# Performance work log

Measured on AMD Instinct MI355X. Metric: run time of the kernel, lower is better.

## Reference

```python
import jax, jax.numpy as jnp
import numpy as np

TEMP = 0.1
EPS = 1e-12  # F.normalize eps


def setup_inputs() -> dict:
    key = jax.random.key(0)
    k1, k2 = jax.random.split(key)
    B, C, N = 8, 128, 4096
    features = jax.random.normal(k1, (B, C, N), dtype=jnp.float32)
    labels_all = jax.random.randint(k2, (B, N), 0, 16, dtype=jnp.int32)
    return {"features": features, "labels_all": labels_all}


def _per_cloud_loss(features_map, labels):
    # features_map: [C, N], labels: [N]
    v = features_map.T  # [N, C]
    v = v / jnp.maximum(jnp.linalg.norm(v, axis=1, keepdims=True), EPS)
    dp = jnp.exp(jnp.matmul(v, v.T) / TEMP)  # [N, N]
    n = dp.shape[0]
    # remove diagonal (dot_products - diag(diagonal))
    dp = dp * (1.0 - jnp.eye(n, dtype=dp.dtype))
    mask = labels[:, None] == labels[None, :]  # [N, N]
    positives = jnp.sum(jnp.where(mask, dp, 0.0), axis=1)
    negatives = jnp.sum(jnp.where(mask, 0.0, dp), axis=1)
    deviation = -jnp.log(positives / (positives + negatives))
    return jnp.mean(deviation)


def reference(features, labels_all):
    # features: [B, C, N], labels_all: [B, N]
    losses = jax.vmap(_per_cloud_loss)(features, labels_all)  # [B]
    return jnp.mean(losses)
```

## Files before the change

### kernel.cpp

```cpp
#include <hip/hip_runtime.h>
#include <hip/hip_bf16.h>
#include <math.h>

#define BATCH 8
#define NPTS 4096
#define CH 128
#define CTG 4
#define ROWS 128
#define CHUNK 32
#define NCHUNK (NPTS / (CTG * CHUNK))
#define NBUF 3

#define SQRT_TEMP_LOG2E 3.79828256f

typedef __attribute__((ext_vector_type(4))) float    f32x4;
typedef __attribute__((ext_vector_type(4))) int      i32x4;
typedef __attribute__((ext_vector_type(8))) short    bf16x8;
typedef __attribute__((ext_vector_type(4))) _Float16 f16x4;

typedef __attribute__((address_space(3))) unsigned int lds_uint;
typedef __attribute__((address_space(1))) const unsigned int gbl_uint;

__device__ __forceinline__ void load_lds16(const void* g, const void* l) {
    __builtin_amdgcn_global_load_lds((gbl_uint*)g, (lds_uint*)l, 16, 0, 0);
}

__device__ __forceinline__ float fast_exp2(float x) {
    return __builtin_amdgcn_exp2f(x);
}

__device__ __forceinline__ f32x4 mfma16(f16x4 a, f16x4 b, f32x4 c) {
#if __has_builtin(__builtin_amdgcn_mfma_f32_16x16x16f16)
    return __builtin_amdgcn_mfma_f32_16x16x16f16(a, b, c, 0, 0, 0);
#else
    f32x4 d = c;
    asm volatile("v_mfma_f32_16x16x16_f16 %0, %1, %2, %0"
                 : "+v"(d) : "v"(a), "v"(b));
    return d;
#endif
}

__global__ __launch_bounds__(256) void normalize_kernel(
    const float* __restrict__ f, __hip_bfloat16* __restrict__ vn,
    float* __restrict__ pos, float* __restrict__ neg, float* __restrict__ out)
{
    const int blk = blockIdx.x;
    const int b = blk >> 6;
    const int n0 = (blk & 63) * 64;
    const int nl = threadIdx.x & 63;
    const int cg = threadIdx.x >> 6;
    const float* base = f + (size_t)b * CH * NPTS + (size_t)(cg * 32) * NPTS
                          + n0 + nl;

    __shared__ float red[4][64];
    __shared__ float scl[64];
    __shared__ short ostage[64 * CH];

    float ss = 0.0f;
    #pragma unroll
    for (int c = 0; c < 32; c++) {
        float v = base[(size_t)c * NPTS];
        ss += v * v;
    }
    red[cg][nl] = ss;
    __syncthreads();
    if (cg == 0) {
        float s = red[0][nl] + red[1][nl] + red[2][nl] + red[3][nl];
        scl[nl] = SQRT_TEMP_LOG2E / fmaxf(sqrtf(s), 1e-12f);
    }
    __syncthreads();
    const float scale = scl[nl];

    #pragma unroll
    for (int k = 0; k < 4; k++) {
        union { __hip_bfloat16 h[8]; uint4 u; } pk;
        #pragma unroll
        for (int j = 0; j < 8; j++) {
            float v = base[(size_t)(k * 8 + j) * NPTS] * scale;
            pk.h[j] = __float2bfloat16(v);
        }
        const int ch8 = cg * 4 + k;
        const int phys = (nl << 4) | (ch8 ^ (nl & 15));
        *(uint4*)&ostage[phys * 8] = pk.u;
    }
    __syncthreads();

    __hip_bfloat16* ob = vn + ((size_t)b * NPTS + n0) * CH;
    const int t = threadIdx.x;
    #pragma unroll
    for (int it = 0; it < 4; it++) {
        const int L = it * 256 + t;
        const int pt = L >> 4, c8 = L & 15;
        const int phys = (pt << 4) | (c8 ^ (pt & 15));
        *(uint4*)(ob + (size_t)L * 8) = *(const uint4*)&ostage[phys * 8];
    }

    if (cg == 0) pos[b * NPTS + n0 + nl] = 0.0f;
    else if (cg == 1) neg[b * NPTS + n0 + nl] = 0.0f;
    if (blk == 0 && t == 0) out[0] = 0.0f;
}

__global__ __launch_bounds__(256, 4) void tile_kernel(
    const __hip_bfloat16* __restrict__ vn, const int* __restrict__ labels,
    float* __restrict__ pos, float* __restrict__ neg)
{
    __shared__ short lB[NBUF][CHUNK * CH];
    __shared__ int labL[NPTS / CTG];

    const int ctg = blockIdx.x, rt = blockIdx.y, b = blockIdx.z;
    const int tid = threadIdx.x;
    const int w = tid >> 6, lane = tid & 63;
    const int lane15 = lane & 15, quad = lane >> 4;

    const int row0 = rt * ROWS;
    const int colbase = ctg * (NPTS / CTG);
    const __hip_bfloat16* vb = vn + (size_t)b * NPTS * CH;
    const int* labb = labels + b * NPTS;

    auto stage = [&](int buf, int chunk) {
        const __hip_bfloat16* Bb = vb + (size_t)(colbase + chunk * CHUNK) * CH;
        #pragma unroll
        for (int i = 0; i < 2; i++) {
            int ldsrow = w * 8 + i * 4;
            int r = ldsrow + quad;
            int g = lane15 ^ (r & 15);
            load_lds16(Bb + (size_t)r * CH + g * 8, &lB[buf][ldsrow * CH]);
        }
    };

    load_lds16(labb + colbase + w * 256 + lane * 4, &labL[w * 256]);

    bf16x8 afrag[2][4];
    int lr[2];
    #pragma unroll
    for (int mi = 0; mi < 2; mi++) {
        const int row_l = w * 32 + mi * 16 + lane15;
        const __hip_bfloat16* Arow = vb + (size_t)(row0 + row_l) * CH;
        #pragma unroll
        for (int ks = 0; ks < 4; ks++)
            afrag[mi][ks] = *(const bf16x8*)(Arow + (ks * 4 + quad) * 8);
        lr[mi] = labb[row0 + row_l];
    }

    stage(0, 0);
    stage(1, 1);

    int vad[2][4];
    #pragma unroll
    for (int ni = 0; ni < 2; ni++)
        #pragma unroll
        for (int ks = 0; ks < 4; ks++)
            vad[ni][ks] = (((ni * 16 + lane15) * CH) +
                           (((ks * 4 + quad) ^ lane15) << 3)) * 2;

    f32x4 qout[2] = {{0.0f, 0.0f, 0.0f, 0.0f}, {0.0f, 0.0f, 0.0f, 0.0f}};
    float ddiag[2] = {0.0f, 0.0f};
    const f32x4 zf = {0.0f, 0.0f, 0.0f, 0.0f};
    f32x4 accA[2][2], accB[2][2];

#define MFMA_PH(BUF_, ACC_)                                                   \
    {                                                                         \
        _Pragma("unroll")                                                     \
        for (int ni = 0; ni < 2; ni++) {                                      \
            bf16x8 bf = *(const bf16x8*)((const char*)(&lB[0][0]) +           \
                         (BUF_) * (CHUNK * CH * 2) + vad[ni][0]);             \
            ACC_[0][ni] = __builtin_amdgcn_mfma_f32_16x16x32_bf16(            \
                bf, afrag[0][0], zf, 0, 0, 0);                                \
            ACC_[1][ni] = __builtin_amdgcn_mfma_f32_16x16x32_bf16(            \
                bf, afrag[1][0], zf, 0, 0, 0);                                \
        }                                                                     \
        _Pragma("unroll")                                                     \
        for (int ks = 1; ks < 4; ks++) {                                      \
            _Pragma("unroll")                                                 \
            for (int ni = 0; ni < 2; ni++) {                                  \
                bf16x8 bf = *(const bf16x8*)((const char*)(&lB[0][0]) +       \
                             (BUF_) * (CHUNK * CH * 2) + vad[ni][ks]);        \
                ACC_[0][ni] = __builtin_amdgcn_mfma_f32_16x16x32_bf16(        \
                    bf, afrag[0][ks], ACC_[0][ni], 0, 0, 0);                  \
                ACC_[1][ni] = __builtin_amdgcn_mfma_f32_16x16x32_bf16(        \
                    bf, afrag[1][ks], ACC_[1][ni], 0, 0, 0);                  \
            }                                                                 \
        }                                                                     \
    }

#define EPI_PH(EC_, ACC_)                                                     \
    {                                                                         \
        _Pragma("unroll")                                                     \
        for (int ni = 0; ni < 2; ni++) {                                      \
            const i32x4 lc = *(const i32x4*)&labL[(EC_) * CHUNK + ni * 16 +   \
                                                  quad * 4];                  \
            f16x4 oh;                                                         \
            _Pragma("unroll")                                                 \
            for (int j = 0; j < 4; j++)                                       \
                oh[j] = (lc[j] == lane15) ? (_Float16)1.0f : (_Float16)0.0f;  \
            const int colblk = colbase + (EC_) * CHUNK + ni * 16;             \
            _Pragma("unroll")                                                 \
            for (int mi = 0; mi < 2; mi++) {                                  \
                f16x4 eh;                                                     \
                _Pragma("unroll")                                             \
                for (int r = 0; r < 4; r++)                                   \
                    eh[r] = (_Float16)fast_exp2(ACC_[mi][ni][r]);             \
                if (colblk == row0 + w * 32 + mi * 16) {    \
                    _Pragma("unroll")                                         \
                    for (int r = 0; r < 4; r++)                               \
                        if (lane15 == quad * 4 + r)                           \
                            ddiag[mi] += (float)eh[r];                        \
                }                                                             \
                qout[mi] = mfma16(oh, eh, qout[mi]);                          \
            }                                                                 \
        }                                                                     \
    }

#define BODY(C_, BUF_, CUR_, PRV_, DOEPI_)                                    \
    {                                                                         \
        __builtin_amdgcn_s_barrier();                                         \
        __builtin_amdgcn_s_setprio(1);                                        \
        MFMA_PH(BUF_, CUR_);                                                  \
        __builtin_amdgcn_s_setprio(0);                                        \
        stage(((BUF_) + 2) % 3, ((C_) + 2) & (NCHUNK - 1));                   \
        if (DOEPI_) { EPI_PH((C_) - 1, PRV_); }                               \
        asm volatile("s_waitcnt vmcnt(2)" ::: "memory");                      \
    }

    asm volatile("s_waitcnt vmcnt(2)" ::: "memory");
    BODY(0, 0, accA, accB, 0);
    #pragma unroll 1
    for (int c = 1; c <= 25; c += 6) {
        BODY(c + 0, 1, accB, accA, 1);
        BODY(c + 1, 2, accA, accB, 1);
        BODY(c + 2, 0, accB, accA, 1);
        BODY(c + 3, 1, accA, accB, 1);
        BODY(c + 4, 2, accB, accA, 1);
        BODY(c + 5, 0, accA, accB, 1);
    }
    __builtin_amdgcn_s_barrier();
    __builtin_amdgcn_s_setprio(1);
    MFMA_PH(1, accB);
    __builtin_amdgcn_s_setprio(0);
    EPI_PH(30, accA);
    EPI_PH(31, accB);

#undef BODY
#undef EPI_PH
#undef MFMA_PH

    #pragma unroll
    for (int mi = 0; mi < 2; mi++) {
        float p = -ddiag[mi], tt = -ddiag[mi];
        #pragma unroll
        for (int r = 0; r < 4; r++) {
            float v = qout[mi][r];
            tt += v;
            p  += (quad * 4 + r == lr[mi]) ? v : 0.0f;
        }
        p  += __shfl_xor(p, 16);   p  += __shfl_xor(p, 32);
        tt += __shfl_xor(tt, 16);  tt += __shfl_xor(tt, 32);
        if (lane < 16) {
            const int row_l = w * 32 + mi * 16 + lane15;
            atomicAdd(&pos[b * NPTS + row0 + row_l], p);
            atomicAdd(&neg[b * NPTS + row0 + row_l], tt - p);
        }
    }
}

__global__ __launch_bounds__(256) void finalize_kernel(
    const float* __restrict__ pos, const float* __restrict__ neg,
    float* __restrict__ out)
{
    int base = blockIdx.x * 1024 + threadIdx.x;
    float acc = 0.0f;
    #pragma unroll
    for (int k = 0; k < 4; k++) {
        int i = base + k * 256;
        float p = pos[i];
        float t = p + neg[i];
        acc += __logf(t / p);
    }
    #pragma unroll
    for (int off = 32; off; off >>= 1) acc += __shfl_down(acc, off);
    __shared__ float red[4];
    if ((threadIdx.x & 63) == 0) red[threadIdx.x >> 6] = acc;
    __syncthreads();
    if (threadIdx.x == 0) {
        float v = red[0] + red[1] + red[2] + red[3];
        atomicAdd(out, v * (1.0f / (BATCH * NPTS)));
    }
}

extern "C" void kernel_launch(void* const* d_in, const int* in_sizes, int n_in,
                              void* d_out, int out_size, void* d_ws, size_t ws_size,
                              hipStream_t stream)
{
    const float* features = (const float*)d_in[0];
    const int*   labels   = (const int*)d_in[1];
    float*       out      = (float*)d_out;

    __hip_bfloat16* vn = (__hip_bfloat16*)d_ws;
    float* pos = (float*)((char*)d_ws + (size_t)BATCH * NPTS * CH * sizeof(__hip_bfloat16));
    float* neg = pos + BATCH * NPTS;

    hipLaunchKernelGGL(normalize_kernel, dim3(512), dim3(256), 0, stream,
                       features, vn, pos, neg, out);
    hipLaunchKernelGGL(tile_kernel, dim3(CTG, NPTS / ROWS, BATCH), dim3(256), 0, stream,
                       vn, labels, pos, neg);
    hipLaunchKernelGGL(finalize_kernel, dim3(32), dim3(256), 0, stream, pos, neg, out);
}
```

Measured before the change: 110.6 us.

## Exploit Gram matrix symmetry by computing only lower-triangular 128x128 tiles

Replaces the full N×N tile sweep with a triangular tile grid, where each block computes one 128×128 tile at or below the diagonal. Off-diagonal tiles also produce column-wise positive/total sums by transposing the exp tile with an identity MFMA and applying the row one-hot labels, then accumulate them through shared memory and atomics. This roughly halves the matmul and exp work, in exchange for extra MFMAs, conversions and atomics in the epilogue and shorter per-block pipelines with more blocks.

```diff
diff --git a/kernel.cpp b/kernel.cpp
--- a/kernel.cpp
+++ b/kernel.cpp
@@ -5,11 +5,8 @@
 #define BATCH 8
 #define NPTS 4096
 #define CH 128
-#define CTG 4
-#define ROWS 128
 #define CHUNK 32
-#define NCHUNK (NPTS / (CTG * CHUNK))
-#define NBUF 3
+#define NTRI 528
 
 #define SQRT_TEMP_LOG2E 3.79828256f
 
@@ -104,21 +101,27 @@
     const __hip_bfloat16* __restrict__ vn, const int* __restrict__ labels,
     float* __restrict__ pos, float* __restrict__ neg)
 {
-    __shared__ short lB[NBUF][CHUNK * CH];
-    __shared__ int labL[NPTS / CTG];
-
-    const int ctg = blockIdx.x, rt = blockIdx.y, b = blockIdx.z;
+    __shared__ short lB[3][CHUNK * CH];
+    __shared__ int labPadC[256];
+    __shared__ int labPadR[256];
+    __shared__ float colp[128], colt[128];
+
+    const int t = blockIdx.x, b = blockIdx.y;
+    int rt = (int)((sqrtf((float)(8 * t + 1)) - 1.0f) * 0.5f);
+    while (rt * (rt + 1) / 2 > t) rt--;
+    while ((rt + 1) * (rt + 2) / 2 <= t) rt++;
+    const int ct = t - rt * (rt + 1) / 2;
+    const bool isdiag = (rt == ct);
+
     const int tid = threadIdx.x;
     const int w = tid >> 6, lane = tid & 63;
     const int lane15 = lane & 15, quad = lane >> 4;
-
-    const int row0 = rt * ROWS;
-    const int colbase = ctg * (NPTS / CTG);
+    const int row0 = rt * 128, col0 = ct * 128;
     const __hip_bfloat16* vb = vn + (size_t)b * NPTS * CH;
     const int* labb = labels + b * NPTS;
 
     auto stage = [&](int buf, int chunk) {
-        const __hip_bfloat16* Bb = vb + (size_t)(colbase + chunk * CHUNK) * CH;
+        const __hip_bfloat16* Bb = vb + (size_t)(col0 + chunk * CHUNK) * CH;
         #pragma unroll
         for (int i = 0; i < 2; i++) {
             int ldsrow = w * 8 + i * 4;
@@ -128,10 +131,10 @@
         }
     };
 
-    load_lds16(labb + colbase + w * 256 + lane * 4, &labL[w * 256]);
+    load_lds16(labb + col0 + (lane & 31) * 4, labPadC);
+    load_lds16(labb + row0 + (lane & 31) * 4, labPadR);
 
     bf16x8 afrag[2][4];
-    int lr[2];
     #pragma unroll
     for (int mi = 0; mi < 2; mi++) {
         const int row_l = w * 32 + mi * 16 + lane15;
@@ -139,11 +142,12 @@
         #pragma unroll
         for (int ks = 0; ks < 4; ks++)
             afrag[mi][ks] = *(const bf16x8*)(Arow + (ks * 4 + quad) * 8);
-        lr[mi] = labb[row0 + row_l];
     }
 
     stage(0, 0);
     stage(1, 1);
+
+    if (tid < 128) { colp[tid] = 0.0f; colt[tid] = 0.0f; }
 
     int vad[2][4];
     #pragma unroll
@@ -152,6 +156,11 @@
         for (int ks = 0; ks < 4; ks++)
             vad[ni][ks] = (((ni * 16 + lane15) * CH) +
                            (((ks * 4 + quad) ^ lane15) << 3)) * 2;
+
+    f16x4 idf;
+    #pragma unroll
+    for (int j = 0; j < 4; j++)
+        idf[j] = (quad * 4 + j == lane15) ? (_Float16)1.0f : (_Float16)0.0f;
 
     f32x4 qout[2] = {{0.0f, 0.0f, 0.0f, 0.0f}, {0.0f, 0.0f, 0.0f, 0.0f}};
     float ddiag[2] = {0.0f, 0.0f};
@@ -187,13 +196,14 @@
     {                                                                         \
         _Pragma("unroll")                                                     \
         for (int ni = 0; ni < 2; ni++) {                                      \
-            const i32x4 lc = *(const i32x4*)&labL[(EC_) * CHUNK + ni * 16 +   \
-                                                  quad * 4];                  \
+            const i32x4 lc = *(const i32x4*)&labPadC[(EC_) * CHUNK + ni * 16  \
+                                                     + quad * 4];             \
             f16x4 oh;                                                         \
             _Pragma("unroll")                                                 \
             for (int j = 0; j < 4; j++)                                       \
                 oh[j] = (lc[j] == lane15) ? (_Float16)1.0f : (_Float16)0.0f;  \
-            const int colblk = colbase + (EC_) * CHUNK + ni * 16;             \
+            const int colblk = col0 + (EC_) * CHUNK + ni * 16;                \
+            f32x4 qc = zf;                                                    \
             _Pragma("unroll")                                                 \
             for (int mi = 0; mi < 2; mi++) {                                  \
                 f16x4 eh;                                                     \
@@ -207,40 +217,69 @@
                             ddiag[mi] += (float)eh[r];                        \
                 }                                                             \
                 qout[mi] = mfma16(oh, eh, qout[mi]);                          \
+                if (!isdiag) {                                                \
+                    f32x4 tr = mfma16(eh, idf, zf);         \
+                    f16x4 trh, ohr;                                           \
+                    _Pragma("unroll")                                         \
+                    for (int r = 0; r < 4; r++)                               \
+                        trh[r] = (_Float16)tr[r];                  \
+                    _Pragma("unroll")                                         \
+                    for (int j = 0; j < 4; j++)                               \
+                        ohr[j] = (lrq[mi][j] == lane15) ? (_Float16)1.0f      \
+                                                        : (_Float16)0.0f;     \
+                    qc = mfma16(ohr, trh, qc);                                \
+                }                                                             \
+            }                                                                 \
+            if (!isdiag) {                                                    \
+                float tc = qc[0] + qc[1] + qc[2] + qc[3];                     \
+                const int cl = labPadC[(EC_) * CHUNK + ni * 16 + lane15];     \
+                float pc = ((cl >> 2) == quad) ? qc[cl & 3] : 0.0f;           \
+                pc += __shfl_xor(pc, 16);  pc += __shfl_xor(pc, 32);          \
+                tc += __shfl_xor(tc, 16);  tc += __shfl_xor(tc, 32);          \
+                if (lane < 16) {                                              \
+                    atomicAdd(&colp[(EC_) * CHUNK + ni * 16 + lane15], pc);   \
+                    atomicAdd(&colt[(EC_) * CHUNK + ni * 16 + lane15], tc);   \
+                }                                                             \
             }                                                                 \
         }                                                                     \
     }
 
-#define BODY(C_, BUF_, CUR_, PRV_, DOEPI_)                                    \
-    {                                                                         \
-        __builtin_amdgcn_s_barrier();                                         \
-        __builtin_amdgcn_s_setprio(1);                                        \
-        MFMA_PH(BUF_, CUR_);                                                  \
-        __builtin_amdgcn_s_setprio(0);                                        \
-        stage(((BUF_) + 2) % 3, ((C_) + 2) & (NCHUNK - 1));                   \
-        if (DOEPI_) { EPI_PH((C_) - 1, PRV_); }                               \
-        asm volatile("s_waitcnt vmcnt(2)" ::: "memory");                      \
-    }
-
     asm volatile("s_waitcnt vmcnt(2)" ::: "memory");
-    BODY(0, 0, accA, accB, 0);
-    #pragma unroll 1
-    for (int c = 1; c <= 25; c += 6) {
-        BODY(c + 0, 1, accB, accA, 1);
-        BODY(c + 1, 2, accA, accB, 1);
-        BODY(c + 2, 0, accB, accA, 1);
-        BODY(c + 3, 1, accA, accB, 1);
-        BODY(c + 4, 2, accB, accA, 1);
-        BODY(c + 5, 0, accA, accB, 1);
-    }
+    int lr[2];
+    i32x4 lrq[2];
+    #pragma unroll
+    for (int mi = 0; mi < 2; mi++) {
+        lr[mi]  = labPadR[w * 32 + mi * 16 + lane15];
+        lrq[mi] = *(const i32x4*)&labPadR[w * 32 + mi * 16 + quad * 4];
+    }
+
+    __builtin_amdgcn_s_barrier();
+    __builtin_amdgcn_s_setprio(1);
+    MFMA_PH(0, accA);
+    __builtin_amdgcn_s_setprio(0);
+    stage(2, 2);
+    asm volatile("s_waitcnt vmcnt(2)" ::: "memory");
     __builtin_amdgcn_s_barrier();
     __builtin_amdgcn_s_setprio(1);
     MFMA_PH(1, accB);
     __builtin_amdgcn_s_setprio(0);
-    EPI_PH(30, accA);
-    EPI_PH(31, accB);
-
-#undef BODY
+    stage(0, 3);
+    EPI_PH(0, accA);
+    asm volatile("s_waitcnt vmcnt(2)" ::: "memory");
+    __builtin_amdgcn_s_barrier();
+    __builtin_amdgcn_s_setprio(1);
+    MFMA_PH(2, accA);
+    __builtin_amdgcn_s_setprio(0);
+    stage(1, 0);
+    EPI_PH(1, accB);
+    asm volatile("s_waitcnt vmcnt(2)" ::: "memory");
+    __builtin_amdgcn_s_barrier();
+    __builtin_amdgcn_s_setprio(1);
+    MFMA_PH(0, accB);
+    __builtin_amdgcn_s_setprio(0);
+    EPI_PH(2, accA);
+    EPI_PH(3, accB);
+
 #undef EPI_PH
 #undef MFMA_PH
 
@@ -261,6 +300,13 @@
             atomicAdd(&neg[b * NPTS + row0 + row_l], tt - p);
         }
     }
+
+    __syncthreads();
+    if (!isdiag && tid < 128) {
+        float p = colp[tid], tt = colt[tid];
+        atomicAdd(&pos[b * NPTS + col0 + tid], p);
+        atomicAdd(&neg[b * NPTS + col0 + tid], tt - p);
+    }
 }
 
 __global__ __launch_bounds__(256) void finalize_kernel(
@@ -301,7 +347,7 @@
 
     hipLaunchKernelGGL(normalize_kernel, dim3(512), dim3(256), 0, stream,
                        features, vn, pos, neg, out);
-    hipLaunchKernelGGL(tile_kernel, dim3(CTG, NPTS / ROWS, BATCH), dim3(256), 0, stream,
+    hipLaunchKernelGGL(tile_kernel, dim3(NTRI, BATCH), dim3(256), 0, stream,
                        vn, labels, pos, neg);
     hipLaunchKernelGGL(finalize_kernel, dim3(32), dim3(256), 0, stream, pos, neg, out);
 }
```

New measurement: 123.5 us. +11.6%, slower.

## Exploit symmetry of the similarity matrix to compute only lower-triangular tiles

Applied to the files above, without the earlier changes.

Each block now handles a pair of 128-column tiles at or below the diagonal of the N×N similarity matrix, using a triangular index mapping over 272 blocks per batch. Off-diagonal tiles also produce column-side positive and negative sums via a transposing MFMA against an identity fragment, accumulated in shared memory and then atomically added to the global row buffers. The intent is to roughly halve the matmul and exp work. In exchange it adds extra MFMAs, shuffles, shared-memory atomics and more global atomics per block, and the per-block work becomes uneven.

```diff
diff --git a/kernel.cpp b/kernel.cpp
--- a/kernel.cpp
+++ b/kernel.cpp
@@ -5,11 +5,8 @@
 #define BATCH 8
 #define NPTS 4096
 #define CH 128
-#define CTG 4
-#define ROWS 128
 #define CHUNK 32
-#define NCHUNK (NPTS / (CTG * CHUNK))
-#define NBUF 3
+#define NPAIR 272
 
 #define SQRT_TEMP_LOG2E 3.79828256f
 
@@ -104,21 +101,34 @@
     const __hip_bfloat16* __restrict__ vn, const int* __restrict__ labels,
     float* __restrict__ pos, float* __restrict__ neg)
 {
-    __shared__ short lB[NBUF][CHUNK * CH];
-    __shared__ int labL[NPTS / CTG];
-
-    const int ctg = blockIdx.x, rt = blockIdx.y, b = blockIdx.z;
+    __shared__ short lB[3][CHUNK * CH];
+    __shared__ int labPadC[256];
+    __shared__ int labPadR[128];
+    __shared__ float colp[256], colt[256];
+
+    const int t = blockIdx.x, b = blockIdx.y;
+    int m = (int)sqrtf((float)t);
+    while ((m + 1) * (m + 1) <= t) m++;
+    while (m * m > t) m--;
+    int rt, k;
+    if (t < m * m + m) { rt = 2 * m - 1; k = t - m * m; }
+    else               { rt = 2 * m;     k = t - m * m - m; }
+    const int ct0 = 2 * k;
+    const bool has2 = (2 * k + 1 <= rt);
+    const bool diagB = (2 * k + 1 == rt);
+    const bool colB = !diagB;
+
     const int tid = threadIdx.x;
     const int w = tid >> 6, lane = tid & 63;
     const int lane15 = lane & 15, quad = lane >> 4;
-
-    const int row0 = rt * ROWS;
-    const int colbase = ctg * (NPTS / CTG);
+    const int row0 = rt * 128;
+    const int col0A = ct0 * 128, col0B = (2 * k + 1) * 128;
     const __hip_bfloat16* vb = vn + (size_t)b * NPTS * CH;
     const int* labb = labels + b * NPTS;
 
-    auto stage = [&](int buf, int chunk) {
-        const __hip_bfloat16* Bb = vb + (size_t)(colbase + chunk * CHUNK) * CH;
+    auto stage = [&](int buf, int c) {
+        const int colg = ((c >= 4) ? col0B : col0A) + (c & 3) * CHUNK;
+        const __hip_bfloat16* Bb = vb + (size_t)colg * CH;
         #pragma unroll
         for (int i = 0; i < 2; i++) {
             int ldsrow = w * 8 + i * 4;
@@ -128,10 +138,13 @@
         }
     };
 
-    load_lds16(labb + colbase + w * 256 + lane * 4, &labL[w * 256]);
+    if (lane < 32) {
+        load_lds16(labb + row0 + lane * 4, labPadR);
+        load_lds16(labb + col0A + lane * 4, labPadC);
+        if (has2) load_lds16(labb + col0B + lane * 4, &labPadC[128]);
+    }
 
     bf16x8 afrag[2][4];
-    int lr[2];
     #pragma unroll
     for (int mi = 0; mi < 2; mi++) {
         const int row_l = w * 32 + mi * 16 + lane15;
@@ -139,11 +152,12 @@
         #pragma unroll
         for (int ks = 0; ks < 4; ks++)
             afrag[mi][ks] = *(const bf16x8*)(Arow + (ks * 4 + quad) * 8);
-        lr[mi] = labb[row0 + row_l];
     }
 
     stage(0, 0);
     stage(1, 1);
+
+    if (tid < 256) { colp[tid] = 0.0f; colt[tid] = 0.0f; }
 
     int vad[2][4];
     #pragma unroll
@@ -152,6 +166,11 @@
         for (int ks = 0; ks < 4; ks++)
             vad[ni][ks] = (((ni * 16 + lane15) * CH) +
                            (((ks * 4 + quad) ^ lane15) << 3)) * 2;
+
+    f16x4 idf;
+    #pragma unroll
+    for (int j = 0; j < 4; j++)
+        idf[j] = (quad * 4 + j == lane15) ? (_Float16)1.0f : (_Float16)0.0f;
 
     f32x4 qout[2] = {{0.0f, 0.0f, 0.0f, 0.0f}, {0.0f, 0.0f, 0.0f, 0.0f}};
     float ddiag[2] = {0.0f, 0.0f};
@@ -183,17 +202,20 @@
         }                                                                     \
     }
 
-#define EPI_PH(EC_, ACC_)                                                     \
+#define EPI_PH(EC_, ACC_, COL_, CB_)                                          \
     {                                                                         \
         _Pragma("unroll")                                                     \
         for (int ni = 0; ni < 2; ni++) {                                      \
-            const i32x4 lc = *(const i32x4*)&labL[(EC_) * CHUNK + ni * 16 +   \
-                                                  quad * 4];                  \
+            const int lidx = (EC_) * CHUNK + ni * 16;                         \
+            const i32x4 lc = *(const i32x4*)&labPadC[lidx + quad * 4];        \
             f16x4 oh;                                                         \
             _Pragma("unroll")                                                 \
             for (int j = 0; j < 4; j++)                                       \
                 oh[j] = (lc[j] == lane15) ? (_Float16)1.0f : (_Float16)0.0f;  \
-            const int colblk = colbase + (EC_) * CHUNK + ni * 16;             \
+            const int colblk = (CB_) + ni * 16;                               \
+            int clm = 0;                                                      \
+            if (COL_) clm = labPadC[lidx + lane15];                           \
+            float pcc = 0.0f, tcc = 0.0f;                                     \
             _Pragma("unroll")                                                 \
             for (int mi = 0; mi < 2; mi++) {                                  \
                 f16x4 eh;                                                     \
@@ -207,40 +229,72 @@
                             ddiag[mi] += (float)eh[r];                        \
                 }                                                             \
                 qout[mi] = mfma16(oh, eh, qout[mi]);                          \
+                if (COL_) {                                                   \
+                    f32x4 tr = mfma16(eh, idf, zf);      \
+                    _Pragma("unroll")                                         \
+                    for (int r = 0; r < 4; r++) {                             \
+                        tcc += tr[r];                                         \
+                        pcc += (lrq[mi][r] == clm) ? tr[r] : 0.0f;            \
+                    }                                                         \
+                }                                                             \
+            }                                                                 \
+            if (COL_) {                                                       \
+                pcc += __shfl_xor(pcc, 16);  pcc += __shfl_xor(pcc, 32);      \
+                tcc += __shfl_xor(tcc, 16);  tcc += __shfl_xor(tcc, 32);      \
+                if (lane < 16) {                                              \
+                    atomicAdd(&colp[lidx + lane15], pcc);                     \
+                    atomicAdd(&colt[lidx + lane15], tcc);                     \
+                }                                                             \
             }                                                                 \
         }                                                                     \
     }
 
-#define BODY(C_, BUF_, CUR_, PRV_, DOEPI_)                                    \
-    {                                                                         \
-        __builtin_amdgcn_s_barrier();                                         \
-        __builtin_amdgcn_s_setprio(1);                                        \
-        MFMA_PH(BUF_, CUR_);                                                  \
-        __builtin_amdgcn_s_setprio(0);                                        \
-        stage(((BUF_) + 2) % 3, ((C_) + 2) & (NCHUNK - 1));                   \
-        if (DOEPI_) { EPI_PH((C_) - 1, PRV_); }                               \
-        asm volatile("s_waitcnt vmcnt(2)" ::: "memory");                      \
-    }
-
-    asm volatile("s_waitcnt vmcnt(2)" ::: "memory");
-    BODY(0, 0, accA, accB, 0);
-    #pragma unroll 1
-    for (int c = 1; c <= 25; c += 6) {
-        BODY(c + 0, 1, accB, accA, 1);
-        BODY(c + 1, 2, accA, accB, 1);
-        BODY(c + 2, 0, accB, accA, 1);
-        BODY(c + 3, 1, accA, accB, 1);
-        BODY(c + 4, 2, accB, accA, 1);
-        BODY(c + 5, 0, accA, accB, 1);
-    }
-    __builtin_amdgcn_s_barrier();
-    __builtin_amdgcn_s_setprio(1);
-    MFMA_PH(1, accB);
-    __builtin_amdgcn_s_setprio(0);
-    EPI_PH(30, accA);
-    EPI_PH(31, accB);
-
-#undef BODY
+#define BAR  __builtin_amdgcn_s_barrier()
+#define P1   __builtin_amdgcn_s_setprio(1)
+#define P0   __builtin_amdgcn_s_setprio(0)
+#define W2   asm volatile("s_waitcnt vmcnt(2)" ::: "memory")
+
+    W2;
+    int lr[2];
+    i32x4 lrq[2];
+    #pragma unroll
+    for (int mi = 0; mi < 2; mi++) {
+        lr[mi]  = labPadR[w * 32 + mi * 16 + lane15];
+        lrq[mi] = *(const i32x4*)&labPadR[w * 32 + mi * 16 + quad * 4];
+    }
+
+    if (has2) {
+        BAR; P1; MFMA_PH(0, accA); P0; stage(2, 2);                        W2;
+        BAR; P1; MFMA_PH(1, accB); P0; stage(0, 3);
+             EPI_PH(0, accA, true, col0A + 0);                             W2;
+        BAR; P1; MFMA_PH(2, accA); P0; stage(1, 4);
+             EPI_PH(1, accB, true, col0A + 32);                            W2;
+        BAR; P1; MFMA_PH(0, accB); P0; stage(2, 5);
+             EPI_PH(2, accA, true, col0A + 64);                            W2;
+        BAR; P1; MFMA_PH(1, accA); P0; stage(0, 6);
+             EPI_PH(3, accB, true, col0A + 96);                            W2;
+        BAR; P1; MFMA_PH(2, accB); P0; stage(1, 7);
+             EPI_PH(4, accA, colB, col0B + 0);                             W2;
+        BAR; P1; MFMA_PH(0, accA); P0; stage(2, 0);
+             EPI_PH(5, accB, colB, col0B + 32);                            W2;
+        BAR; P1; MFMA_PH(1, accB); P0;
+             EPI_PH(6, accA, colB, col0B + 64);
+             EPI_PH(7, accB, colB, col0B + 96);
+    } else {
+        BAR; P1; MFMA_PH(0, accA); P0; stage(2, 2);                        W2;
+        BAR; P1; MFMA_PH(1, accB); P0; stage(0, 3);
+             EPI_PH(0, accA, false, col0A + 0);                            W2;
+        BAR; P1; MFMA_PH(2, accA); P0; stage(1, 0);
+             EPI_PH(1, accB, false, col0A + 32);                           W2;
+        BAR; P1; MFMA_PH(0, accB); P0;
+             EPI_PH(2, accA, false, col0A + 64);
+             EPI_PH(3, accB, false, col0A + 96);
+    }
+
+#undef W2
+#undef P0
+#undef P1
+#undef BAR
 #undef EPI_PH
 #undef MFMA_PH
 
@@ -259,6 +313,20 @@
             const int row_l = w * 32 + mi * 16 + lane15;
             atomicAdd(&pos[b * NPTS + row0 + row_l], p);
             atomicAdd(&neg[b * NPTS + row0 + row_l], tt - p);
+        }
+    }
+
+    __syncthreads();
+    if (has2) {
+        if (tid < 128) {
+            float p = colp[tid], tt = colt[tid];
+            atomicAdd(&pos[b * NPTS + col0A + tid], p);
+            atomicAdd(&neg[b * NPTS + col0A + tid], tt - p);
+        } else if (colB) {
+            const int c = tid - 128;
+            float p = colp[tid], tt = colt[tid];
+            atomicAdd(&pos[b * NPTS + col0B + c], p);
+            atomicAdd(&neg[b * NPTS + col0B + c], tt - p);
         }
     }
 }
@@ -301,7 +369,7 @@
 
     hipLaunchKernelGGL(normalize_kernel, dim3(512), dim3(256), 0, stream,
                        features, vn, pos, neg, out);
-    hipLaunchKernelGGL(tile_kernel, dim3(CTG, NPTS / ROWS, BATCH), dim3(256), 0, stream,
+    hipLaunchKernelGGL(tile_kernel, dim3(NPAIR, BATCH), dim3(256), 0, stream,
                        vn, labels, pos, neg);
     hipLaunchKernelGGL(finalize_kernel, dim3(32), dim3(256), 0, stream, pos, neg, out);
 }
```

Result: slower. 124.6 us (+12.7%).

## Replace LDS triple-buffered B staging with direct global loads into registers

Applied to the files above, without the earlier changes.

Removes the shared-memory triple buffer and the async global-to-LDS staging pipeline. Each wave now reads its B fragments straight from global memory (L2/L1 cached) into registers every chunk, and no longer needs per-chunk barriers. The software-pipelined MFMA/epilogue interleave becomes a simple loop unrolled by two. The aim is to cut LDS traffic and barrier stalls, at the cost of redundant global loads across the four waves and exposed load latency.

```diff
diff --git a/kernel.cpp b/kernel.cpp
--- a/kernel.cpp
+++ b/kernel.cpp
@@ -9,7 +9,6 @@
 #define ROWS 128
 #define CHUNK 32
 #define NCHUNK (NPTS / (CTG * CHUNK))
-#define NBUF 3
 
 #define SQRT_TEMP_LOG2E 3.79828256f
 
@@ -17,13 +16,6 @@
 typedef __attribute__((ext_vector_type(4))) int      i32x4;
 typedef __attribute__((ext_vector_type(8))) short    bf16x8;
 typedef __attribute__((ext_vector_type(4))) _Float16 f16x4;
-
-typedef __attribute__((address_space(3))) unsigned int lds_uint;
-typedef __attribute__((address_space(1))) const unsigned int gbl_uint;
-
-__device__ __forceinline__ void load_lds16(const void* g, const void* l) {
-    __builtin_amdgcn_global_load_lds((gbl_uint*)g, (lds_uint*)l, 16, 0, 0);
-}
 
 __device__ __forceinline__ float fast_exp2(float x) {
     return __builtin_amdgcn_exp2f(x);
@@ -104,7 +96,6 @@
     const __hip_bfloat16* __restrict__ vn, const int* __restrict__ labels,
     float* __restrict__ pos, float* __restrict__ neg)
 {
-    __shared__ short lB[NBUF][CHUNK * CH];
     __shared__ int labL[NPTS / CTG];
 
     const int ctg = blockIdx.x, rt = blockIdx.y, b = blockIdx.z;
@@ -117,18 +108,7 @@
     const __hip_bfloat16* vb = vn + (size_t)b * NPTS * CH;
     const int* labb = labels + b * NPTS;
 
-    auto stage = [&](int buf, int chunk) {
-        const __hip_bfloat16* Bb = vb + (size_t)(colbase + chunk * CHUNK) * CH;
-        #pragma unroll
-        for (int i = 0; i < 2; i++) {
-            int ldsrow = w * 8 + i * 4;
-            int r = ldsrow + quad;
-            int g = lane15 ^ (r & 15);
-            load_lds16(Bb + (size_t)r * CH + g * 8, &lB[buf][ldsrow * CH]);
-        }
-    };
-
-    load_lds16(labb + colbase + w * 256 + lane * 4, &labL[w * 256]);
+    ((i32x4*)labL)[tid] = ((const i32x4*)(labb + colbase))[tid];
 
     bf16x8 afrag[2][4];
     int lr[2];
@@ -141,108 +121,68 @@
             afrag[mi][ks] = *(const bf16x8*)(Arow + (ks * 4 + quad) * 8);
         lr[mi] = labb[row0 + row_l];
     }
-
-    stage(0, 0);
-    stage(1, 1);
-
-    int vad[2][4];
-    #pragma unroll
-    for (int ni = 0; ni < 2; ni++)
-        #pragma unroll
-        for (int ks = 0; ks < 4; ks++)
-            vad[ni][ks] = (((ni * 16 + lane15) * CH) +
-                           (((ks * 4 + quad) ^ lane15) << 3)) * 2;
+    __syncthreads();
+
+    const __hip_bfloat16* vbl = vb + (size_t)(colbase + lane15) * CH + quad * 8;
 
     f32x4 qout[2] = {{0.0f, 0.0f, 0.0f, 0.0f}, {0.0f, 0.0f, 0.0f, 0.0f}};
     float ddiag[2] = {0.0f, 0.0f};
     const f32x4 zf = {0.0f, 0.0f, 0.0f, 0.0f};
-    f32x4 accA[2][2], accB[2][2];
-
-#define MFMA_PH(BUF_, ACC_)                                                   \
-    {                                                                         \
-        _Pragma("unroll")                                                     \
-        for (int ni = 0; ni < 2; ni++) {                                      \
-            bf16x8 bf = *(const bf16x8*)((const char*)(&lB[0][0]) +           \
-                         (BUF_) * (CHUNK * CH * 2) + vad[ni][0]);             \
-            ACC_[0][ni] = __builtin_amdgcn_mfma_f32_16x16x32_bf16(            \
-                bf, afrag[0][0], zf, 0, 0, 0);                                \
-            ACC_[1][ni] = __builtin_amdgcn_mfma_f32_16x16x32_bf16(            \
-                bf, afrag[1][0], zf, 0, 0, 0);                                \
-        }                                                                     \
-        _Pragma("unroll")                                                     \
-        for (int ks = 1; ks < 4; ks++) {                                      \
-            _Pragma("unroll")                                                 \
-            for (int ni = 0; ni < 2; ni++) {                                  \
-                bf16x8 bf = *(const bf16x8*)((const char*)(&lB[0][0]) +       \
-                             (BUF_) * (CHUNK * CH * 2) + vad[ni][ks]);        \
-                ACC_[0][ni] = __builtin_amdgcn_mfma_f32_16x16x32_bf16(        \
-                    bf, afrag[0][ks], ACC_[0][ni], 0, 0, 0);                  \
-                ACC_[1][ni] = __builtin_amdgcn_mfma_f32_16x16x32_bf16(        \
-                    bf, afrag[1][ks], ACC_[1][ni], 0, 0, 0);                  \
-            }                                                                 \
-        }                                                                     \
-    }
-
-#define EPI_PH(EC_, ACC_)                                                     \
-    {                                                                         \
-        _Pragma("unroll")                                                     \
-        for (int ni = 0; ni < 2; ni++) {                                      \
-            const i32x4 lc = *(const i32x4*)&labL[(EC_) * CHUNK + ni * 16 +   \
-                                                  quad * 4];                  \
-            f16x4 oh;                                                         \
-            _Pragma("unroll")                                                 \
-            for (int j = 0; j < 4; j++)                                       \
-                oh[j] = (lc[j] == lane15) ? (_Float16)1.0f : (_Float16)0.0f;  \
-            const int colblk = colbase + (EC_) * CHUNK + ni * 16;             \
-            _Pragma("unroll")                                                 \
-            for (int mi = 0; mi < 2; mi++) {                                  \
-                f16x4 eh;                                                     \
-                _Pragma("unroll")                                             \
-                for (int r = 0; r < 4; r++)                                   \
-                    eh[r] = (_Float16)fast_exp2(ACC_[mi][ni][r]);             \
-                if (colblk == row0 + w * 32 + mi * 16) {    \
-                    _Pragma("unroll")                                         \
-                    for (int r = 0; r < 4; r++)                               \
-                        if (lane15 == quad * 4 + r)                           \
-                            ddiag[mi] += (float)eh[r];                        \
-                }                                                             \
-                qout[mi] = mfma16(oh, eh, qout[mi]);                          \
-            }                                                                 \
-        }                                                                     \
-    }
-
-#define BODY(C_, BUF_, CUR_, PRV_, DOEPI_)                                    \
-    {                                                                         \
-        __builtin_amdgcn_s_barrier();                                         \
-        __builtin_amdgcn_s_setprio(1);                                        \
-        MFMA_PH(BUF_, CUR_);                                                  \
-        __builtin_amdgcn_s_setprio(0);                                        \
-        stage(((BUF_) + 2) % 3, ((C_) + 2) & (NCHUNK - 1));                   \
-        if (DOEPI_) { EPI_PH((C_) - 1, PRV_); }                               \
-        asm volatile("s_waitcnt vmcnt(2)" ::: "memory");                      \
-    }
-
-    asm volatile("s_waitcnt vmcnt(2)" ::: "memory");
-    BODY(0, 0, accA, accB, 0);
-    #pragma unroll 1
-    for (int c = 1; c <= 25; c += 6) {
-        BODY(c + 0, 1, accB, accA, 1);
-        BODY(c + 1, 2, accA, accB, 1);
-        BODY(c + 2, 0, accB, accA, 1);
-        BODY(c + 3, 1, accA, accB, 1);
-        BODY(c + 4, 2, accB, accA, 1);
-        BODY(c + 5, 0, accA, accB, 1);
-    }
-    __builtin_amdgcn_s_barrier();
-    __builtin_amdgcn_s_setprio(1);
-    MFMA_PH(1, accB);
-    __builtin_amdgcn_s_setprio(0);
-    EPI_PH(30, accA);
-    EPI_PH(31, accB);
-
-#undef BODY
-#undef EPI_PH
-#undef MFMA_PH
+
+    #pragma unroll 2
+    for (int c = 0; c < NCHUNK; c++) {
+        const __hip_bfloat16* Bc = vbl + (size_t)c * (CHUNK * CH);
+        bf16x8 bf[2][4];
+        #pragma unroll
+        for (int ni = 0; ni < 2; ni++)
+            #pragma unroll
+            for (int ks = 0; ks < 4; ks++)
+                bf[ni][ks] = *(const bf16x8*)(Bc + ni * 16 * CH + ks * 32);
+
+        f32x4 acc[2][2];
+        __builtin_amdgcn_s_setprio(1);
+        #pragma unroll
+        for (int ni = 0; ni < 2; ni++) {
+            acc[0][ni] = __builtin_amdgcn_mfma_f32_16x16x32_bf16(
+                bf[ni][0], afrag[0][0], zf, 0, 0, 0);
+            acc[1][ni] = __builtin_amdgcn_mfma_f32_16x16x32_bf16(
+                bf[ni][0], afrag[1][0], zf, 0, 0, 0);
+        }
+        #pragma unroll
+        for (int ks = 1; ks < 4; ks++)
+            #pragma unroll
+            for (int ni = 0; ni < 2; ni++) {
+                acc[0][ni] = __builtin_amdgcn_mfma_f32_16x16x32_bf16(
+                    bf[ni][ks], afrag[0][ks], acc[0][ni], 0, 0, 0);
+                acc[1][ni] = __builtin_amdgcn_mfma_f32_16x16x32_bf16(
+                    bf[ni][ks], afrag[1][ks], acc[1][ni], 0, 0, 0);
+            }
+        __builtin_amdgcn_s_setprio(0);
+
+        #pragma unroll
+        for (int ni = 0; ni < 2; ni++) {
+            const i32x4 lc = *(const i32x4*)&labL[c * CHUNK + ni * 16 + quad * 4];
+            f16x4 oh;
+            #pragma unroll
+            for (int j = 0; j < 4; j++)
+                oh[j] = (lc[j] == lane15) ? (_Float16)1.0f : (_Float16)0.0f;
+            const int colblk = colbase + c * CHUNK + ni * 16;
+            #pragma unroll
+            for (int mi = 0; mi < 2; mi++) {
+                f16x4 eh;
+                #pragma unroll
+                for (int r = 0; r < 4; r++)
+                    eh[r] = (_Float16)fast_exp2(acc[mi][ni][r]);
+                if (colblk == row0 + w * 32 + mi * 16) {
+                    #pragma unroll
+                    for (int r = 0; r < 4; r++)
+                        if (lane15 == quad * 4 + r)
+                            ddiag[mi] += (float)eh[r];
+                }
+                qout[mi] = mfma16(oh, eh, qout[mi]);
+            }
+        }
+    }
 
     #pragma unroll
     for (int mi = 0; mi < 2; mi++) {
```

Result: slower. 186.6 us (+68.7%).
